# Kernel tuning notes

Measured on AMD Instinct MI355X. Metric: run time of the kernel, lower is better.

## Reference

```python
import jax, jax.numpy as jnp
import numpy as np

D_MODEL = 1024
N_HEADS = 16
HEAD_DIM = D_MODEL // N_HEADS
D_FF = 4 * D_MODEL
SEQ = 2048
BATCH = 2
EPS = 1e-6


def setup_inputs() -> dict:
    key = jax.random.key(0)
    ks = jax.random.split(key, 8)
    s = 0.02
    return {
        "x": jax.random.normal(ks[0], (SEQ, BATCH, D_MODEL), dtype=jnp.float32),
        "g1": jnp.ones((D_MODEL,), dtype=jnp.float32),                # norm1 weight
        "g2": jnp.ones((D_MODEL,), dtype=jnp.float32),                # norm2 weight
        "Wq": jax.random.normal(ks[1], (N_HEADS, D_MODEL, HEAD_DIM), dtype=jnp.float32) * s,
        "Wk": jax.random.normal(ks[2], (N_HEADS, D_MODEL, HEAD_DIM), dtype=jnp.float32) * s,
        "Wv": jax.random.normal(ks[3], (N_HEADS, D_MODEL, HEAD_DIM), dtype=jnp.float32) * s,
        "Wo": jax.random.normal(ks[4], (D_MODEL, D_MODEL), dtype=jnp.float32) * s,
        "W1": jax.random.normal(ks[5], (D_MODEL, D_FF), dtype=jnp.float32) * s,
        "W2": jax.random.normal(ks[6], (D_FF, D_MODEL), dtype=jnp.float32) * s,
    }


def _rmsnorm(x, g):
    rms = jnp.sqrt(jnp.mean(x * x, axis=-1, keepdims=True) + EPS)
    return g * (x / rms)


def _block(x, g1, g2, Wq, Wk, Wv, Wo, W1, W2):
    S = x.shape[0]
    scale = HEAD_DIM ** -0.5
    # --- attention (pre-norm) ---
    h = _rmsnorm(x, g1)                              # (S, B, D)
    Q = jnp.einsum('sbd,hdk->bhsk', h, Wq)           # (B, H, S, K)
    K = jnp.einsum('sbd,hdk->bhsk', h, Wk)
    V = jnp.einsum('sbd,hdk->bhsk', h, Wv)
    scores = jnp.einsum('bhsk,bhtk->bhst', Q, K) * scale
    causal = jnp.tril(jnp.ones((S, S), dtype=bool))
    scores = jnp.where(causal, scores, -jnp.inf)
    attn = jax.nn.softmax(scores, axis=-1)
    ctx = jnp.einsum('bhst,bhtk->sbhk', attn, V)     # heads concatenated in order
    ctx = ctx.reshape(S, x.shape[1], D_MODEL)
    x = x + ctx @ Wo
    # --- FFN (pre-norm) ---
    h2 = _rmsnorm(x, g2)
    x = x + jax.nn.silu(h2 @ W1) @ W2
    return x


def reference(x, g1, g2, Wq, Wk, Wv, Wo, W1, W2):
    return _block(x, g1, g2, Wq, Wk, Wv, Wo, W1, W2)
```

## Files before the change

kernel.cpp:

```cpp
#include <hip/hip_runtime.h>

typedef unsigned short u16;
typedef __bf16 bf16x8 __attribute__((ext_vector_type(8)));
typedef u16 u16x8 __attribute__((ext_vector_type(8)));
typedef u16 u16x4 __attribute__((ext_vector_type(4)));
typedef float f32x4 __attribute__((ext_vector_type(4)));

__device__ __forceinline__ u16 f2bf(float f) {
    union { float f; unsigned int u; } x; x.f = f;
    unsigned int r = x.u + 0x7FFFu + ((x.u >> 16) & 1u);
    return (u16)(r >> 16);
}

__device__ __forceinline__ u16 f2bf_hw(float f) {
    union { __bf16 b; u16 u; } x; x.b = (__bf16)f; return x.u;
}

__device__ __forceinline__ void gload_lds16(const u16* g, u16* l) {
    __builtin_amdgcn_global_load_lds(
        (const __attribute__((address_space(1))) unsigned int*)g,
        (__attribute__((address_space(3))) unsigned int*)l, 16, 0, 0);
}


__device__ __forceinline__ void transT_body(
    const float* __restrict__ in, u16* __restrict__ out, int R, int C,
    int bx, int by, float T[64][65], int tid)
{
    const int r0 = bx * 64, c0 = by * 64;
    const int tr = tid >> 4;
    const int tc = (tid & 15) * 4;
    #pragma unroll
    for (int k = 0; k < 4; k++) {
        f32x4 v = *(const f32x4*)(in + (size_t)(c0 + 16 * k + tr) * R + r0 + tc);
        T[16 * k + tr][tc]     = v[0];
        T[16 * k + tr][tc + 1] = v[1];
        T[16 * k + tr][tc + 2] = v[2];
        T[16 * k + tr][tc + 3] = v[3];
    }
    __syncthreads();
    #pragma unroll
    for (int k = 0; k < 4; k++) {
        const int rl = 16 * k + tr;
        u16x4 o;
        #pragma unroll
        for (int i = 0; i < 4; i++) o[i] = f2bf(T[tc + i][rl]);
        *(u16x4*)(out + (size_t)(r0 + rl) * C + c0 + tc) = o;
    }
}

__global__ __launch_bounds__(256) void prep_k(
    const float* __restrict__ Wq, const float* __restrict__ Wk,
    const float* __restrict__ Wv, const float* __restrict__ Wo,
    const float* __restrict__ W1, const float* __restrict__ W2,
    const float* __restrict__ x, const float* __restrict__ g1,
    u16* __restrict__ bqkvT, u16* __restrict__ woT,
    u16* __restrict__ w1T, u16* __restrict__ w2T, u16* __restrict__ h1)
{
    __shared__ float T[64][65];
    const int id = blockIdx.x;
    const int tid = threadIdx.x;

    if (id < 768) {
        const int bx = id & 15, y = id >> 4;
        const int d0 = bx * 64;
        const int wsel = y >> 4, h = y & 15;
        const float* W = (wsel == 0) ? Wq : (wsel == 1) ? Wk : Wv;
        const float scale = (wsel == 0) ? 0.125f * 1.44269504088896f : 1.0f;
        const int tr = tid >> 4;
        const int tc = (tid & 15) * 4;
        #pragma unroll
        for (int k = 0; k < 4; k++) {
            f32x4 v = *(const f32x4*)(W + (size_t)h * 65536 + (size_t)(d0 + 16 * k + tr) * 64 + tc);
            T[16 * k + tr][tc]     = v[0];
            T[16 * k + tr][tc + 1] = v[1];
            T[16 * k + tr][tc + 2] = v[2];
            T[16 * k + tr][tc + 3] = v[3];
        }
        __syncthreads();
        #pragma unroll
        for (int k = 0; k < 4; k++) {
            const int kk = 16 * k + tr;
            u16x4 o;
            #pragma unroll
            for (int i = 0; i < 4; i++) o[i] = f2bf(T[tc + i][kk] * scale);
            *(u16x4*)(bqkvT + (size_t)(wsel * 1024 + h * 64 + kk) * 1024 + d0 + tc) = o;
        }
    } else if (id < 1024) {
        const int id2 = id - 768;
        transT_body(Wo, woT, 1024, 1024, id2 & 15, id2 >> 4, T, tid);
    } else if (id < 2048) {
        const int id3 = id - 1024;
        transT_body(W1, w1T, 4096, 1024, id3 & 63, id3 >> 6, T, tid);
    } else if (id < 3072) {
        const int id4 = id - 2048;
        transT_body(W2, w2T, 1024, 4096, id4 & 15, id4 >> 4, T, tid);
    } else {
        const int row = id - 3072;
        const float* xr = x + (size_t)row * 1024;
        f32x4 v = *(const f32x4*)(xr + tid * 4);
        float ss = v[0] * v[0] + v[1] * v[1] + v[2] * v[2] + v[3] * v[3];
        #pragma unroll
        for (int off = 32; off > 0; off >>= 1) ss += __shfl_down(ss, off);
        float* red = &T[0][0];
        if ((tid & 63) == 0) red[tid >> 6] = ss;
        __syncthreads();
        float sum = red[0] + red[1] + red[2] + red[3];
        float rinv = rsqrtf(sum * (1.0f / 1024.0f) + 1e-6f);
        f32x4 gv = *(const f32x4*)(g1 + tid * 4);
        u16x4 o;
        #pragma unroll
        for (int i = 0; i < 4; i++) o[i] = f2bf(v[i] * gv[i] * rinv);
        *(u16x4*)(h1 + (size_t)row * 1024 + tid * 4) = o;
    }
}

__global__ __launch_bounds__(256) void vtrans_k(const u16* __restrict__ qkv, u16* __restrict__ vT)
{
    __shared__ u16 T[64][72];
    const int bh = blockIdx.x, b = bh >> 4, h = bh & 15;
    const int s0 = blockIdx.y * 64;
    const int tid = threadIdx.x;
    const int r = tid >> 2, c0 = (tid & 3) * 16;
    const u16* src = qkv + ((size_t)((s0 + r) * 2 + b)) * 3072 + 2048 + h * 64 + c0;
    *(u16x8*)&T[r][c0] = *(const u16x8*)src;
    *(u16x8*)&T[r][c0 + 8] = *(const u16x8*)(src + 8);
    __syncthreads();
    u16x8 o0, o1;
    #pragma unroll
    for (int i = 0; i < 8; i++) o0[i] = T[c0 + i][r];
    #pragma unroll
    for (int i = 0; i < 8; i++) o1[i] = T[c0 + 8 + i][r];
    u16* dst = vT + (size_t)(bh * 64 + r) * 2048 + s0 + c0;
    *(u16x8*)dst = o0;
    *(u16x8*)(dst + 8) = o1;
}

__global__ __launch_bounds__(256) void addred_norm_k(
    const float* __restrict__ res, const float* __restrict__ p0,
    const float* __restrict__ p1, const float* __restrict__ g,
    float* __restrict__ xout, u16* __restrict__ hout)
{
    const int row = blockIdx.x;
    const int tid = threadIdx.x;
    const size_t base = (size_t)row * 1024 + tid * 4;
    f32x4 a = *(const f32x4*)(res + base);
    f32x4 b = *(const f32x4*)(p0 + base);
    f32x4 c = *(const f32x4*)(p1 + base);
    f32x4 o = a + b + c;
    *(f32x4*)(xout + base) = o;
    float ss = o[0] * o[0] + o[1] * o[1] + o[2] * o[2] + o[3] * o[3];
    #pragma unroll
    for (int off = 32; off > 0; off >>= 1) ss += __shfl_down(ss, off);
    __shared__ float red[4];
    if ((tid & 63) == 0) red[tid >> 6] = ss;
    __syncthreads();
    float sum = red[0] + red[1] + red[2] + red[3];
    float rinv = rsqrtf(sum * (1.0f / 1024.0f) + 1e-6f);
    f32x4 gv = *(const f32x4*)(g + tid * 4);
    u16x4 hv;
    #pragma unroll
    for (int i = 0; i < 4; i++) hv[i] = f2bf(o[i] * gv[i] * rinv);
    *(u16x4*)(hout + base) = hv;
}

__global__ __launch_bounds__(256) void addred4_k(
    const float* __restrict__ xm, const float* __restrict__ a0,
    const float* __restrict__ a1, const float* __restrict__ a2,
    const float* __restrict__ a3, float* __restrict__ out)
{
    int i = (blockIdx.x * 256 + threadIdx.x) * 4;
    f32x4 v = *(const f32x4*)(xm + i);
    v = v + *(const f32x4*)(a0 + i);
    v = v + *(const f32x4*)(a1 + i);
    v = v + *(const f32x4*)(a2 + i);
    v = v + *(const f32x4*)(a3 + i);
    *(f32x4*)(out + i) = v;
}

template <int MODE>
__global__ __launch_bounds__(256) void gemm_bt_k(
    const u16* __restrict__ A, const u16* __restrict__ BT,
    u16* __restrict__ outB, float* __restrict__ outF, const float* __restrict__ res,
    int M, int N, int K, int klen)
{
    __shared__ u16 As[2][128 * 64];
    __shared__ u16 Bs[2][128 * 64];
    const int tid = threadIdx.x;
    const int lane = tid & 63, w = tid >> 6;
    const int wm = w >> 1, wn = w & 1;
    const int quad = lane >> 4, l15 = lane & 15;
    const int bid = blockIdx.x + gridDim.x * blockIdx.y;
    const int bj = bid >> 3;
    const int m0 = ((bid & 7) * 4 + (bj & 3)) * 128;
    const int n0 = (bj >> 2) * 128;
    const int kbeg = blockIdx.z * klen;

    f32x4 acc[4][4] = {};

    const int srow = (w << 3) + (lane >> 3);
    const int swz = ((lane & 7) ^ (lane >> 3)) << 3;
    const u16* aA = A + (size_t)(m0 + srow) * K + kbeg + swz;
    const u16* aB = BT + (size_t)(n0 + srow) * K + kbeg + swz;
    const int wo = w * 512;
    const int rsw = (l15 & 7) << 3;

    #pragma unroll
    for (int c = 0; c < 4; c++) {
        gload_lds16(aA + (size_t)(c * 32) * K, &As[0][0] + c * 2048 + wo);
        gload_lds16(aB + (size_t)(c * 32) * K, &Bs[0][0] + c * 2048 + wo);
    }

    int cur = 0;
    for (int k0 = 0; k0 < klen; k0 += 64) {
        __syncthreads();
        if (k0 + 64 < klen) {
            #pragma unroll
            for (int c = 0; c < 4; c++) {
                gload_lds16(aA + (size_t)(c * 32) * K + k0 + 64, &As[cur ^ 1][0] + c * 2048 + wo);
                gload_lds16(aB + (size_t)(c * 32) * K + k0 + 64, &Bs[cur ^ 1][0] + c * 2048 + wo);
            }
        }
        const u16* AB = &As[cur][0];
        const u16* BB = &Bs[cur][0];
        #pragma unroll
        for (int kh = 0; kh < 2; kh++) {
            const int cb = ((kh * 4 + quad) << 3);
            bf16x8 af[4], bfr[4];
            #pragma unroll
            for (int i = 0; i < 4; i++)
                af[i] = *(const bf16x8*)(AB + (wm * 64 + i * 16 + l15) * 64 + (cb ^ rsw));
            #pragma unroll
            for (int j = 0; j < 4; j++)
                bfr[j] = *(const bf16x8*)(BB + (wn * 64 + j * 16 + l15) * 64 + (cb ^ rsw));
            #pragma unroll
            for (int i = 0; i < 4; i++)
                #pragma unroll
                for (int j = 0; j < 4; j++)
                    acc[i][j] = __builtin_amdgcn_mfma_f32_16x16x32_bf16(af[i], bfr[j], acc[i][j], 0, 0, 0);
        }
        cur ^= 1;
    }

    float* outFz = (MODE == 3) ? outF + (size_t)blockIdx.z * M * N : outF;
    #pragma unroll
    for (int i = 0; i < 4; i++) {
        const int row = m0 + wm * 64 + i * 16 + quad * 4;
        #pragma unroll
        for (int j = 0; j < 4; j++) {
            const int col = n0 + wn * 64 + j * 16 + l15;
            #pragma unroll
            for (int r = 0; r < 4; r++) {
                const size_t idx = (size_t)(row + r) * N + col;
                float v = acc[i][j][r];
                if (MODE == 0) {
                    outB[idx] = f2bf_hw(v);
                } else if (MODE == 1) {
                    outF[idx] = res[idx] + v;
                } else if (MODE == 2) {
                    float e = exp2f(v * -1.44269504088896f);
                    outB[idx] = f2bf_hw(v * __builtin_amdgcn_rcpf(1.0f + e));
                } else {
                    outFz[idx] = v;
                }
            }
        }
    }
}

#define MMQ(FH, AS, BS) \
    { _Pragma("unroll") \
      for (int i_ = 0; i_ < 4; i_++) { \
        acc[(FH)*4+i_][0] = __builtin_amdgcn_mfma_f32_16x16x32_bf16(AS[i_], BS[0], acc[(FH)*4+i_][0], 0, 0, 0); \
        acc[(FH)*4+i_][1] = __builtin_amdgcn_mfma_f32_16x16x32_bf16(AS[i_], BS[1], acc[(FH)*4+i_][1], 0, 0, 0); \
        acc[(FH)*4+i_][2] = __builtin_amdgcn_mfma_f32_16x16x32_bf16(AS[i_], BS[2], acc[(FH)*4+i_][2], 0, 0, 0); \
        acc[(FH)*4+i_][3] = __builtin_amdgcn_mfma_f32_16x16x32_bf16(AS[i_], BS[3], acc[(FH)*4+i_][3], 0, 0, 0); \
      } }

#define SBAR   __builtin_amdgcn_s_barrier()
#define FENCE  asm volatile("" ::: "memory")

template <int MODE>
__global__ __launch_bounds__(512, 2) void gemm8p_k(
    const u16* __restrict__ A, const u16* __restrict__ BT,
    u16* __restrict__ outB, float* __restrict__ q0, float* __restrict__ q1,
    float* __restrict__ q2, float* __restrict__ q3,
    int N, int K, int klen)
{
    __shared__ u16 sm[65536];
    const int tid = threadIdx.x;
    const int lane = tid & 63, w = tid >> 6;
    const int l15 = lane & 15, quad = lane >> 4;
    const int wm = w >> 2, wn = w & 3;

    const int nwg = gridDim.x;
    const int bid = blockIdx.x;
    const int s = (bid & 7) * (nwg >> 3) + (bid >> 3);
    const int m0 = (s & 15) * 256;
    const int n0 = (s >> 4) * 256;
    const int kbeg = blockIdx.z * klen;
    const int nT = klen >> 6;

    const int srow = w * 16 + (lane >> 2);
    const int scol = (((lane & 3) ^ ((lane >> 3) & 3)) << 3);
    const u16* gA = A + (size_t)(m0 + srow) * K + kbeg + scol;
    const u16* gB = BT + (size_t)(n0 + srow) * K + kbeg + scol;
    const size_t cstep = (size_t)128 * K;

    const int rswz = ((quad ^ ((l15 >> 1) & 3)) << 3);
    const int raoff = (wm * 128 + l15) * 32 + rswz;
    const int rboff = (wn * 64 + l15) * 32 + rswz;

    f32x4 acc[8][4] = {};

    auto stA = [&](int t, int kh) {
        u16* d = sm + (t & 1) * 32768 + kh * 8192 + w * 512;
        const u16* g = gA + (size_t)(t * 64 + kh * 32);
        gload_lds16(g, d);
        gload_lds16(g + cstep, d + 4096);
    };
    auto stB = [&](int t, int kh) {
        u16* d = sm + (t & 1) * 32768 + 16384 + kh * 8192 + w * 512;
        const u16* g = gB + (size_t)(t * 64 + kh * 32);
        gload_lds16(g, d);
        gload_lds16(g + cstep, d + 4096);
    };
    auto rdB = [&](int buf, int kh, bf16x8* b) {
        const u16* p = sm + buf * 32768 + 16384 + kh * 8192 + rboff;
        b[0] = *(const bf16x8*)(p);
        b[1] = *(const bf16x8*)(p + 512);
        b[2] = *(const bf16x8*)(p + 1024);
        b[3] = *(const bf16x8*)(p + 1536);
    };
    auto rdA = [&](int buf, int kh, int fh, bf16x8* a) {
        const u16* p = sm + buf * 32768 + kh * 8192 + fh * 2048 + raoff;
        a[0] = *(const bf16x8*)(p);
        a[1] = *(const bf16x8*)(p + 512);
        a[2] = *(const bf16x8*)(p + 1024);
        a[3] = *(const bf16x8*)(p + 1536);
    };

    stA(0, 0); stB(0, 0); stA(0, 1); stB(0, 1);
    if (nT > 1) {
        stA(1, 0); stB(1, 0);
        asm volatile("s_waitcnt vmcnt(4)" ::: "memory");
    } else {
        asm volatile("s_waitcnt vmcnt(0)" ::: "memory");
    }
    SBAR; FENCE;

    for (int t = 0; t < nT; t++) {
        const int buf = t & 1;
        bf16x8 a[4], b[4];
        rdA(buf, 0, 0, a); rdB(buf, 0, b);
        if (t + 1 < nT) stA(t + 1, 1);
        SBAR; FENCE;
        __builtin_amdgcn_s_setprio(1);
        MMQ(0, a, b)
        __builtin_amdgcn_s_setprio(0);
        SBAR; FENCE;
        rdA(buf, 0, 1, a);
        if (t + 1 < nT) stB(t + 1, 1);
        SBAR; FENCE;
        __builtin_amdgcn_s_setprio(1);
        MMQ(1, a, b)
        __builtin_amdgcn_s_setprio(0);
        SBAR; FENCE;
        rdA(buf, 1, 0, a); rdB(buf, 1, b);
        if (t + 2 < nT) stA(t + 2, 0);
        SBAR; FENCE;
        __builtin_amdgcn_s_setprio(1);
        MMQ(0, a, b)
        __builtin_amdgcn_s_setprio(0);
        SBAR; FENCE;
        rdA(buf, 1, 1, a);
        if (t + 2 < nT) {
            stB(t + 2, 0);
            asm volatile("s_waitcnt vmcnt(4)" ::: "memory");
        } else {
            asm volatile("s_waitcnt vmcnt(0)" ::: "memory");
        }
        SBAR; FENCE;
        __builtin_amdgcn_s_setprio(1);
        MMQ(1, a, b)
        __builtin_amdgcn_s_setprio(0);
        SBAR; FENCE;
    }

    float* po = nullptr;
    if (MODE == 3)
        po = (blockIdx.z == 0) ? q0 : (blockIdx.z == 1) ? q1 : (blockIdx.z == 2) ? q2 : q3;
    #pragma unroll
    for (int mf = 0; mf < 8; mf++) {
        const int row = m0 + wm * 128 + mf * 16 + quad * 4;
        #pragma unroll
        for (int nf = 0; nf < 4; nf++) {
            const int col = n0 + wn * 64 + nf * 16 + l15;
            #pragma unroll
            for (int r = 0; r < 4; r++) {
                const size_t idx = (size_t)(row + r) * N + col;
                const float v = acc[mf][nf][r];
                if (MODE == 0) {
                    outB[idx] = f2bf_hw(v);
                } else if (MODE == 2) {
                    float e = exp2f(v * -1.44269504088896f);
                    outB[idx] = f2bf_hw(v * __builtin_amdgcn_rcpf(1.0f + e));
                } else {
                    po[idx] = v;
                }
            }
        }
    }
}

__global__ __launch_bounds__(256, 4) void attn_k(const u16* __restrict__ qkv,
                                                 const u16* __restrict__ vT,
                                                 u16* __restrict__ ctx)
{
    const int bh = blockIdx.x;
    const int qt = 31 - (int)blockIdx.y;
    const int b = bh >> 4, h = bh & 15;
    const int q0 = qt * 64;
    const int tid = threadIdx.x;
    const int lane = tid & 63, w = tid >> 6;
    const int quad = lane >> 4, l15 = lane & 15;

    __shared__ u16 Ks[2][4096];
    __shared__ u16 Vs[2][4096];

    const int q = q0 + 16 * w + l15;
    const u16* qrow = qkv + ((size_t)(q * 2 + b)) * 3072 + h * 64;
    const bf16x8 aq0 = *(const bf16x8*)(qrow + quad * 8);
    const bf16x8 aq1 = *(const bf16x8*)(qrow + 32 + quad * 8);

    bf16x8 ones;
    #pragma unroll
    for (int i = 0; i < 8; i++) ones[i] = (__bf16)1.0f;

    const int kr = (w << 3) + (lane >> 3);
    const int swz = ((lane & 7) ^ (lane >> 3)) << 3;
    const int ldsoff = w * 512;
    const u16* kbase0 = qkv + ((size_t)(kr * 2 + b)) * 3072 + 1024 + h * 64 + swz;
    const u16* kbase1 = kbase0 + (size_t)32 * 2 * 3072;
    const u16* vrow0 = vT + (size_t)(bh * 64 + kr) * 2048 + swz;
    const u16* vrow1 = vrow0 + (size_t)32 * 2048;

    const int sl = (l15 & 3) | ((l15 & 4) << 1) | ((l15 & 8) >> 1);
    const int rswk = (sl & 7) << 3;
    const int rswv = (l15 & 7) << 3;
    const int sq = ((quad & 1) << 1) | (quad >> 1);
    const int qloc = 16 * w + l15;

    f32x4 o[4] = {};
    f32x4 accl = {};

    gload_lds16(kbase0, &Ks[0][0] + ldsoff);
    gload_lds16(kbase1, &Ks[0][0] + 2048 + ldsoff);
    gload_lds16(vrow0, &Vs[0][0] + ldsoff);
    gload_lds16(vrow1, &Vs[0][0] + 2048 + ldsoff);

    int cur = 0;
    for (int t0 = 0; t0 <= q0; t0 += 64) {
        __syncthreads();
        if (t0 + 64 <= q0) {
            const size_t go = (size_t)(t0 + 64) * 2 * 3072;
            u16* KB = &Ks[cur ^ 1][0];
            u16* VB = &Vs[cur ^ 1][0];
            gload_lds16(kbase0 + go, KB + ldsoff);
            gload_lds16(kbase1 + go, KB + 2048 + ldsoff);
            gload_lds16(vrow0 + (t0 + 64), VB + ldsoff);
            gload_lds16(vrow1 + (t0 + 64), VB + 2048 + ldsoff);
        }
        const u16* KB = &Ks[cur][0];
        const u16* VB = &Vs[cur][0];

        f32x4 s[4];
        __builtin_amdgcn_s_setprio(1);
        #pragma unroll
        for (int tg = 0; tg < 4; tg++) {
            const u16* kb = KB + (16 * tg + sl) * 64;
            bf16x8 ak0 = *(const bf16x8*)(kb + ((quad << 3) ^ rswk));
            bf16x8 ak1 = *(const bf16x8*)(kb + (((quad + 4) << 3) ^ rswk));
            f32x4 c = {};
            c = __builtin_amdgcn_mfma_f32_16x16x32_bf16(ak0, aq0, c, 0, 0, 0);
            c = __builtin_amdgcn_mfma_f32_16x16x32_bf16(ak1, aq1, c, 0, 0, 0);
            s[tg] = c;
        }
        __builtin_amdgcn_s_setprio(0);

        if (t0 == q0) {
            #pragma unroll
            for (int tg = 0; tg < 4; tg++)
                #pragma unroll
                for (int r = 0; r < 4; r++)
                    if ((16 * tg + 4 * sq + r) > qloc) s[tg][r] = -1e30f;
        }

        unsigned dd[4][2];
        #pragma unroll
        for (int tg = 0; tg < 4; tg++) {
            float e0 = exp2f(s[tg][0]), e1 = exp2f(s[tg][1]);
            float e2 = exp2f(s[tg][2]), e3 = exp2f(s[tg][3]);
            asm("v_cvt_pk_bf16_f32 %0, %1, %2" : "=v"(dd[tg][0]) : "v"(e0), "v"(e1));
            asm("v_cvt_pk_bf16_f32 %0, %1, %2" : "=v"(dd[tg][1]) : "v"(e2), "v"(e3));
        }
        unsigned x0 = dd[0][0], y0 = dd[1][0];
        asm volatile("v_permlane32_swap_b32 %0, %1" : "+v"(x0), "+v"(y0));
        unsigned x1 = dd[0][1], y1 = dd[1][1];
        asm volatile("v_permlane32_swap_b32 %0, %1" : "+v"(x1), "+v"(y1));
        unsigned x2 = dd[2][0], y2 = dd[3][0];
        asm volatile("v_permlane32_swap_b32 %0, %1" : "+v"(x2), "+v"(y2));
        unsigned x3 = dd[2][1], y3 = dd[3][1];
        asm volatile("v_permlane32_swap_b32 %0, %1" : "+v"(x3), "+v"(y3));

        union { unsigned u[4]; bf16x8 v; } pu0, pu1;
        pu0.u[0] = x0; pu0.u[1] = x1; pu0.u[2] = y0; pu0.u[3] = y1;
        pu1.u[0] = x2; pu1.u[1] = x3; pu1.u[2] = y2; pu1.u[3] = y3;
        const bf16x8 pf0 = pu0.v, pf1 = pu1.v;

        __builtin_amdgcn_s_setprio(1);
        accl = __builtin_amdgcn_mfma_f32_16x16x32_bf16(ones, pf0, accl, 0, 0, 0);
        accl = __builtin_amdgcn_mfma_f32_16x16x32_bf16(ones, pf1, accl, 0, 0, 0);
        #pragma unroll
        for (int i = 0; i < 4; i++) {
            const u16* vb = VB + (i * 16 + l15) * 64;
            bf16x8 av0 = *(const bf16x8*)(vb + ((quad << 3) ^ rswv));
            bf16x8 av1 = *(const bf16x8*)(vb + (((quad + 4) << 3) ^ rswv));
            o[i] = __builtin_amdgcn_mfma_f32_16x16x32_bf16(av0, pf0, o[i], 0, 0, 0);
            o[i] = __builtin_amdgcn_mfma_f32_16x16x32_bf16(av1, pf1, o[i], 0, 0, 0);
        }
        __builtin_amdgcn_s_setprio(0);
        cur ^= 1;
    }

    const float linv = 1.0f / accl[0];
    #pragma unroll
    for (int i = 0; i < 4; i++) {
        u16x4 ov;
        #pragma unroll
        for (int r = 0; r < 4; r++) ov[r] = f2bf_hw(o[i][r] * linv);
        *(u16x4*)(ctx + ((size_t)(q * 2 + b)) * 1024 + h * 64 + i * 16 + quad * 4) = ov;
    }
}

extern "C" void kernel_launch(void* const* d_in, const int* in_sizes, int n_in,
                              void* d_out, int out_size, void* d_ws, size_t ws_size,
                              hipStream_t stream)
{
    (void)in_sizes; (void)n_in; (void)out_size; (void)ws_size;
    const float* x  = (const float*)d_in[0];
    const float* g1 = (const float*)d_in[1];
    const float* g2 = (const float*)d_in[2];
    const float* Wq = (const float*)d_in[3];
    const float* Wk = (const float*)d_in[4];
    const float* Wv = (const float*)d_in[5];
    const float* Wo = (const float*)d_in[6];
    const float* W1 = (const float*)d_in[7];
    const float* W2 = (const float*)d_in[8];
    float* out = (float*)d_out;

    char* ws = (char*)d_ws;
    u16*   bqkvT = (u16*)(ws);
    u16*   woT   = (u16*)(ws + 6291456);
    u16*   w1T   = (u16*)(ws + 8388608);
    u16*   w2T   = (u16*)(ws + 16777216);
    u16*   h1    = (u16*)(ws + 25165824);
    u16*   qkvB  = (u16*)(ws + 33554432);
    u16*   vT    = (u16*)(ws + 25165824);
    u16*   ctxB  = (u16*)(ws + 58720256);
    float* xmid  = (float*)(ws + 41943040);
    u16*   h2    = (u16*)(ws + 83886080);
    u16*   actB  = (u16*)(ws + 92274688);
    float* partO = (float*)(ws + 92274688);
    float* p0 = (float*)(ws);
    float* p1 = (float*)(ws + 25165824);
    float* p2 = (float*)(ws + 58720256);
    float* p3 = (float*)(ws + 75497472);

    prep_k<<<7168, 256, 0, stream>>>(Wq, Wk, Wv, Wo, W1, W2, x, g1,
                                     bqkvT, woT, w1T, w2T, h1);

    gemm8p_k<0><<<dim3(192, 1, 1), 512, 0, stream>>>(h1, bqkvT, qkvB,
                                                     nullptr, nullptr, nullptr, nullptr,
                                                     3072, 1024, 1024);
    vtrans_k<<<dim3(32, 32), 256, 0, stream>>>(qkvB, vT);
    attn_k<<<dim3(32, 32), 256, 0, stream>>>(qkvB, vT, ctxB);

    gemm_bt_k<3><<<dim3(8, 32, 2), 256, 0, stream>>>(ctxB, woT, nullptr, partO, nullptr,
                                                     4096, 1024, 1024, 512);
    addred_norm_k<<<4096, 256, 0, stream>>>(x, partO, partO + 4096 * 1024, g2, xmid, h2);

    gemm8p_k<2><<<dim3(256, 1, 1), 512, 0, stream>>>(h2, w1T, actB,
                                                     nullptr, nullptr, nullptr, nullptr,
                                                     4096, 1024, 1024);
    gemm8p_k<3><<<dim3(64, 1, 4), 512, 0, stream>>>(actB, w2T, nullptr,
                                                    p0, p1, p2, p3,
                                                    1024, 4096, 1024);
    addred4_k<<<4096 * 1024 / 1024, 256, 0, stream>>>(xmid, p0, p1, p2, p3, out);
}
```

Baseline: 312.2 us.

## Switch GEMM LDS tiles to full 64-wide K rows with XOR swizzle

Changes the LDS staging layout of the 256x256 GEMM from two 32-column K-halves into single 64-column rows with an 8-way XOR swizzle. Each tile is now loaded with four 16-byte global_load_lds calls per thread. The prefetch schedule is simplified: the whole next tile is issued in the first half of the iteration, and the loop waits for vmcnt(0) instead of keeping loads two half-steps ahead. This gives wider contiguous global rows and possibly fewer LDS bank conflicts, at the cost of a shallower prefetch pipeline and full drains each iteration.

```diff
diff --git a/kernel.cpp b/kernel.cpp
--- a/kernel.cpp
+++ b/kernel.cpp
@@ -301,85 +301,70 @@
     const int kbeg = blockIdx.z * klen;
     const int nT = klen >> 6;
 
-    const int srow = w * 16 + (lane >> 2);
-    const int scol = (((lane & 3) ^ ((lane >> 3) & 3)) << 3);
+    const int srow = w * 8 + (lane >> 3);
+    const int scol = ((lane & 7) ^ (lane >> 3)) << 3;
     const u16* gA = A + (size_t)(m0 + srow) * K + kbeg + scol;
     const u16* gB = BT + (size_t)(n0 + srow) * K + kbeg + scol;
-    const size_t cstep = (size_t)128 * K;
-
-    const int rswz = ((quad ^ ((l15 >> 1) & 3)) << 3);
-    const int raoff = (wm * 128 + l15) * 32 + rswz;
-    const int rboff = (wn * 64 + l15) * 32 + rswz;
+    const size_t rstep = (size_t)64 * K;
+
+    const int rsw = (l15 & 7) << 3;
 
     f32x4 acc[8][4] = {};
 
-    auto stA = [&](int t, int kh) {
-        u16* d = sm + (t & 1) * 32768 + kh * 8192 + w * 512;
-        const u16* g = gA + (size_t)(t * 64 + kh * 32);
-        gload_lds16(g, d);
-        gload_lds16(g + cstep, d + 4096);
+    auto stA = [&](int t) {
+        u16* d = sm + (t & 1) * 32768 + w * 512;
+        const u16* g = gA + (size_t)(t * 64);
+        #pragma unroll
+        for (int c = 0; c < 4; c++) gload_lds16(g + c * rstep, d + c * 4096);
     };
-    auto stB = [&](int t, int kh) {
-        u16* d = sm + (t & 1) * 32768 + 16384 + kh * 8192 + w * 512;
-        const u16* g = gB + (size_t)(t * 64 + kh * 32);
-        gload_lds16(g, d);
-        gload_lds16(g + cstep, d + 4096);
+    auto stB = [&](int t) {
+        u16* d = sm + (t & 1) * 32768 + 16384 + w * 512;
+        const u16* g = gB + (size_t)(t * 64);
+        #pragma unroll
+        for (int c = 0; c < 4; c++) gload_lds16(g + c * rstep, d + c * 4096);
+    };
+    auto rdA = [&](int buf, int kh, int fh, bf16x8* a) {
+        const u16* p = sm + buf * 32768 + (wm * 128 + fh * 64 + l15) * 64
+                       + (((kh * 4 + quad) << 3) ^ rsw);
+        #pragma unroll
+        for (int i = 0; i < 4; i++) a[i] = *(const bf16x8*)(p + i * 1024);
     };
     auto rdB = [&](int buf, int kh, bf16x8* b) {
-        const u16* p = sm + buf * 32768 + 16384 + kh * 8192 + rboff;
-        b[0] = *(const bf16x8*)(p);
-        b[1] = *(const bf16x8*)(p + 512);
-        b[2] = *(const bf16x8*)(p + 1024);
-        b[3] = *(const bf16x8*)(p + 1536);
+        const u16* p = sm + buf * 32768 + 16384 + (wn * 64 + l15) * 64
+                       + (((kh * 4 + quad) << 3) ^ rsw);
+        #pragma unroll
+        for (int j = 0; j < 4; j++) b[j] = *(const bf16x8*)(p + j * 1024);
     };
-    auto rdA = [&](int buf, int kh, int fh, bf16x8* a) {
-        const u16* p = sm + buf * 32768 + kh * 8192 + fh * 2048 + raoff;
-        a[0] = *(const bf16x8*)(p);
-        a[1] = *(const bf16x8*)(p + 512);
-        a[2] = *(const bf16x8*)(p + 1024);
-        a[3] = *(const bf16x8*)(p + 1536);
-    };
-
-    stA(0, 0); stB(0, 0); stA(0, 1); stB(0, 1);
-    if (nT > 1) {
-        stA(1, 0); stB(1, 0);
-        asm volatile("s_waitcnt vmcnt(4)" ::: "memory");
-    } else {
-        asm volatile("s_waitcnt vmcnt(0)" ::: "memory");
-    }
+
+    stA(0); stB(0);
+    asm volatile("s_waitcnt vmcnt(0)" ::: "memory");
     SBAR; FENCE;
 
     for (int t = 0; t < nT; t++) {
         const int buf = t & 1;
         bf16x8 a[4], b[4];
         rdA(buf, 0, 0, a); rdB(buf, 0, b);
-        if (t + 1 < nT) stA(t + 1, 1);
+        if (t + 1 < nT) stA(t + 1);
         SBAR; FENCE;
         __builtin_amdgcn_s_setprio(1);
         MMQ(0, a, b)
         __builtin_amdgcn_s_setprio(0);
         SBAR; FENCE;
         rdA(buf, 0, 1, a);
-        if (t + 1 < nT) stB(t + 1, 1);
+        if (t + 1 < nT) stB(t + 1);
         SBAR; FENCE;
         __builtin_amdgcn_s_setprio(1);
         MMQ(1, a, b)
         __builtin_amdgcn_s_setprio(0);
         SBAR; FENCE;
         rdA(buf, 1, 0, a); rdB(buf, 1, b);
-        if (t + 2 < nT) stA(t + 2, 0);
         SBAR; FENCE;
         __builtin_amdgcn_s_setprio(1);
         MMQ(0, a, b)
         __builtin_amdgcn_s_setprio(0);
         SBAR; FENCE;
         rdA(buf, 1, 1, a);
-        if (t + 2 < nT) {
-            stB(t + 2, 0);
-            asm volatile("s_waitcnt vmcnt(4)" ::: "memory");
-        } else {
-            asm volatile("s_waitcnt vmcnt(0)" ::: "memory");
-        }
+        asm volatile("s_waitcnt vmcnt(0)" ::: "memory");
         SBAR; FENCE;
         __builtin_amdgcn_s_setprio(1);
         MMQ(1, a, b)
```

Measured after the change: 315.4 us. No clear change (+1.0%).
